# Kernel tuning notes

Hardware: AMD Instinct MI355X
Metric: run time of the kernel (lower is better)

## Reference

```python
import jax, jax.numpy as jnp
import numpy as np

NUM_BLOCKS = 8
WIDTH = 512
HIDDEN_SIZE_FACTOR = 1
HARD_THRESH_FRAC = 1.0
BLOCK_SIZE = WIDTH // NUM_BLOCKS


def setup_inputs() -> dict:
    key = jax.random.key(0)
    k_x, k1, k2, k3, k4 = jax.random.split(key, 5)
    B, L, P, C = 4, 2048, WIDTH, 8
    bs = BLOCK_SIZE
    hf = HIDDEN_SIZE_FACTOR
    scale = 1.0 / (bs * bs * hf)
    x = jax.random.normal(k_x, (B, L, P, C), dtype=jnp.float32)
    w1 = scale * jax.random.uniform(k1, (2, NUM_BLOCKS, bs, bs * hf), dtype=jnp.float32)
    b1 = scale * jax.random.uniform(k2, (2, NUM_BLOCKS, bs * hf), dtype=jnp.float32)
    w2 = scale * jax.random.uniform(k3, (2, NUM_BLOCKS, bs * hf, bs), dtype=jnp.float32)
    b2 = scale * jax.random.uniform(k4, (2, NUM_BLOCKS, bs), dtype=jnp.float32)
    return {"x": x, "w1": w1, "b1": b1, "w2": w2, "b2": b2}


def _gelu(v):
    # torch nn.GELU default is the exact (erf) variant
    return jax.nn.gelu(v, approximate=False)


def reference(x, w1, b1, w2, b2):
    B, L, P, C = x.shape
    nb, bs = NUM_BLOCKS, BLOCK_SIZE
    # rfft along L (norm='ortho'); complex64
    xf = jnp.fft.rfft(x, axis=1, norm="ortho")          # (B, Lf, P, C)
    Lf = xf.shape[1]
    xf = jnp.transpose(xf, (0, 1, 3, 2))                  # (B, Lf, C, P)
    xf = xf.reshape(B, Lf, C, nb, bs)                     # split P into blocks
    kept = int(Lf * HARD_THRESH_FRAC)
    xr, xi = jnp.real(xf[:, :kept]), jnp.imag(xf[:, :kept])
    # block-diagonal complex 2-layer MLP
    mm = lambda a, w: jnp.einsum("blcni,nio->blcno", a, w)
    o1r = _gelu(mm(xr, w1[0]) - mm(xi, w1[1]) + b1[0])
    o1i = _gelu(mm(xi, w1[0]) + mm(xr, w1[1]) + b1[1])
    o2r = mm(o1r, w2[0]) - mm(o1i, w2[1]) + b2[0]
    o2i = mm(o1i, w2[0]) + mm(o1r, w2[1]) + b2[1]
    # zero-pad the thresholded modes (no-op when kept == Lf)
    pad = Lf - kept
    if pad > 0:
        z = jnp.zeros((B, pad, C, nb, bs), dtype=o2r.dtype)
        o2r = jnp.concatenate([o2r, z], axis=1)
        o2i = jnp.concatenate([o2i, z], axis=1)
    xc = (o2r + 1j * o2i).reshape(B, Lf, C, P)
    out = jnp.fft.irfft(xc, n=L, axis=1, norm="ortho")  # (B, L, C, P)
    out = jnp.transpose(out, (0, 1, 3, 2))               # (B, L, P, C)
    return (out + x).astype(x.dtype)
```

## Files before the change

kernel.cpp:

```cpp
#include <hip/hip_runtime.h>
#include <hip/hip_bf16.h>

typedef unsigned short u16;
typedef unsigned int   u32;
typedef __bf16 bf16x8 __attribute__((ext_vector_type(8)));
typedef float  f32x4  __attribute__((ext_vector_type(4)));
typedef u32    u32x2  __attribute__((ext_vector_type(2)));

#define KPAD 1088
#define SEQ  1104
#define PI_F 3.14159265358979323846f
#define WAVE_FENCE() asm volatile("s_waitcnt lgkmcnt(0)" ::: "memory")

__device__ __forceinline__ u16 f2bf(float f){
    u32 u = __float_as_uint(f);
    return (u16)((u + 0x7FFFu + ((u >> 16) & 1u)) >> 16);
}
__device__ __forceinline__ float bf2f(u16 v){ return __uint_as_float(((u32)v) << 16); }
__device__ __forceinline__ int zmap2(int e){ return e + (e >> 4) + 4*(e >> 8); }

__device__ __forceinline__ int sig(int k){
    k &= 1023;
    int a = (k >> 6) + (((k >> 2) & 15) << 4) + ((k & 3) << 8);
    return zmap2(a);
}

__device__ __forceinline__ float2 cmul(float2 a, float2 b){
    return make_float2(a.x*b.x - a.y*b.y, a.x*b.y + a.y*b.x);
}
__device__ __forceinline__ void fft4v(float2& x0, float2& x1, float2& x2, float2& x3){
    float2 t0 = make_float2(x0.x+x2.x, x0.y+x2.y);
    float2 t1 = make_float2(x0.x-x2.x, x0.y-x2.y);
    float2 t2 = make_float2(x1.x+x3.x, x1.y+x3.y);
    float2 t3 = make_float2(x1.x-x3.x, x1.y-x3.y);
    x0 = make_float2(t0.x+t2.x, t0.y+t2.y);
    x2 = make_float2(t0.x-t2.x, t0.y-t2.y);
    x1 = make_float2(t1.x+t3.y, t1.y-t3.x);
    x3 = make_float2(t1.x-t3.y, t1.y+t3.x);
}
__device__ __forceinline__ void fft16(float2 a[16]){
    #pragma unroll
    for (int u1 = 0; u1 < 4; ++u1) fft4v(a[u1], a[u1+4], a[u1+8], a[u1+12]);
    const float Cq = 0.70710678118654752f;
    const float c1 = 0.92387953251128674f, s1 = 0.38268343236508977f;
    a[5]  = cmul(a[5],  make_float2(c1, -s1));
    a[6]  = cmul(a[6],  make_float2(Cq, -Cq));
    a[7]  = cmul(a[7],  make_float2(s1, -c1));
    a[9]  = cmul(a[9],  make_float2(Cq, -Cq));
    a[10] = cmul(a[10], make_float2(0.0f, -1.0f));
    a[11] = cmul(a[11], make_float2(-Cq, -Cq));
    a[13] = cmul(a[13], make_float2(s1, -c1));
    a[14] = cmul(a[14], make_float2(-Cq, -Cq));
    a[15] = cmul(a[15], make_float2(-c1, s1));
    #pragma unroll
    for (int ja = 0; ja < 4; ++ja) fft4v(a[4*ja], a[4*ja+1], a[4*ja+2], a[4*ja+3]);
}

__device__ __forceinline__ void fft_stepB_wave(float2* Z, int lane){
    int nA = lane & 15, jv = lane >> 4;
    float2 a[16];
    #pragma unroll
    for (int u = 0; u < 16; ++u) a[u] = Z[zmap2(nA + 16*u + 256*jv)];
    fft16(a);
    float s_, c_;
    __sincosf(-2.0f*PI_F*(float)(nA*jv)*(1.0f/1024.0f), &s_, &c_);
    float2 tw = make_float2(c_, s_);
    __sincosf(-2.0f*PI_F*(float)nA*(1.0f/256.0f), &s_, &c_);
    float2 st = make_float2(c_, s_);
    #pragma unroll
    for (int ju = 0; ju < 16; ++ju){
        Z[zmap2(nA + 16*ju + 256*jv)] = cmul(a[((ju&3)<<2)|(ju>>2)], tw);
        tw = cmul(tw, st);
    }
}
__device__ __forceinline__ void fft_stepC_wave(float2* Z, int lane){
    int ju = (lane & 63) >> 2, jv = lane & 3;
    float2 a[16];
    #pragma unroll
    for (int nA = 0; nA < 16; ++nA) a[nA] = Z[zmap2(nA + 16*ju + 256*jv)];
    fft16(a);
    #pragma unroll
    for (int kO = 0; kO < 16; ++kO)
        Z[zmap2(kO + 16*ju + 256*jv)] = a[((kO&3)<<2)|(kO>>2)];
}

__global__ __launch_bounds__(256) void prep_w(const float* __restrict__ w1,
                                              const float* __restrict__ w2,
                                              u16* __restrict__ WSW){
    int gid = blockIdx.x * 256 + threadIdx.x;
    int qd = gid >> 12;
    int t  = qd & 1;
    int n  = (qd >> 1) & 7;
    int l  = qd >> 4;
    int rr = gid & 4095;
    int o  = rr >> 6;
    int k  = rr & 63;
    const float* w = l ? w2 : w1;
    WSW[gid] = f2bf(w[((size_t)(t*8 + n)*64 + k)*64 + o]);
}


__device__ __forceinline__ u16 unpack_one(const float2* Zc, int k, int pl, float sf){
    float2 Zk = Zc[sig(k)], Zm = Zc[sig(1024 - k)];
    float sn_, cs_; __sincosf(PI_F*(float)k*(1.0f/1024.0f), &sn_, &cs_);
    float Er=0.5f*(Zk.x+Zm.x), Ei=0.5f*(Zk.y-Zm.y);
    float Dr=0.5f*(Zk.x-Zm.x), Di=0.5f*(Zk.y+Zm.y);
    float Xr = Er + cs_*Di - sn_*Dr;
    float Xi = Ei - sn_*Di - cs_*Dr;
    return f2bf((pl ? Xi : Xr) * sf);
}

__global__ __launch_bounds__(256) void fwd_fft(const float* __restrict__ X,
                                               u16* __restrict__ S){
    __shared__ float2 Zs[4*SEQ];
    int tid = threadIdx.x;
    int blk = blockIdx.x;
    int b = blk >> 10;
    int q = blk & 1023;
    int m8 = q & 7, tq = q >> 3;
    int Q = (tq >> 2)*8 + m8, s4 = tq & 3;
    int col0 = Q*16 + s4*4;
    int p  = col0 >> 3;
    int c0 = col0 & 7;
    int n  = p >> 6, pl_ = p & 63;
    int wave = tid >> 6, lane = tid & 63;

    float2 zz[4][4];
    #pragma unroll
    for (int v = 0; v < 4; ++v){
        int pi = tid + 256*v;
        size_t base = ((size_t)(b*2048 + 2*pi)*512 + p)*8 + c0;
        f32x4 ve = *(const f32x4*)(X + base);
        f32x4 vo = *(const f32x4*)(X + base + 4096);
        #pragma unroll
        for (int s = 0; s < 4; ++s) zz[v][s] = make_float2(ve[s], vo[s]);
    }
    {
        int u = (tid >> 4) & 15;
        float s_, c_;
        __sincosf(-2.0f*PI_F*(float)u*(1.0f/64.0f), &s_, &c_);
        float2 tw1 = make_float2(c_, s_);
        float2 tw2 = cmul(tw1, tw1);
        float2 tw3 = cmul(tw2, tw1);
        #pragma unroll
        for (int s = 0; s < 4; ++s){
            float2 x0 = zz[0][s], x1 = zz[1][s], x2 = zz[2][s], x3 = zz[3][s];
            fft4v(x0, x1, x2, x3);
            float2* Z = Zs + s*SEQ;
            Z[zmap2(tid)]     = x0;
            Z[zmap2(tid+256)] = cmul(x1, tw1);
            Z[zmap2(tid+512)] = cmul(x2, tw2);
            Z[zmap2(tid+768)] = cmul(x3, tw3);
        }
    }
    __syncthreads();
    float2* Z = Zs + wave*SEQ;
    fft_stepB_wave(Z, lane);
    WAVE_FENCE();
    fft_stepC_wave(Z, lane);
    WAVE_FENCE();
    const float sf = 0.02209708691207961f;
    int pl = lane >> 5, tr = lane & 31;
    u16* rp = S + (size_t)((((b*8 + (c0+wave))*8 + n)*2 + pl)*64 + pl_)*KPAD;
    for (int kk = tr*2; kk <= 1024; kk += 64){
        u16 w0 = unpack_one(Z, kk, pl, sf);
        if (kk < 1024){
            u16 w1 = unpack_one(Z, kk+1, pl, sf);
            *(u32*)(rp + kk) = (u32)w0 | ((u32)w1 << 16);
        } else {
            rp[kk] = w0;
        }
    }
}

__device__ __forceinline__ bf16x8 fetchB(const u16* mat, int o64, int k64, bool neg){
    const u32x2* pb = (const u32x2*)(mat + o64*68 + k64);
    u32x2 lo = pb[0], hi = pb[1];
    union { u32 u[4]; bf16x8 v; } bt;
    bt.u[0]=lo.x; bt.u[1]=lo.y; bt.u[2]=hi.x; bt.u[3]=hi.y;
    if (neg){ bt.u[0]^=0x80008000u; bt.u[1]^=0x80008000u; bt.u[2]^=0x80008000u; bt.u[3]^=0x80008000u; }
    return bt.v;
}
__device__ __forceinline__ bf16x8 loadU16x8(const u16* pp){
    union { u32 u[4]; bf16x8 v; } t;
    const u32* qq = (const u32*)pp;
    t.u[0]=qq[0]; t.u[1]=qq[1]; t.u[2]=qq[2]; t.u[3]=qq[3];
    return t.v;
}

__global__ __launch_bounds__(256) void mlp_kernel(const u16* __restrict__ WSW,
                                                  const float* __restrict__ b1,
                                                  const float* __restrict__ b2,
                                                  u16* __restrict__ S){
    __shared__ __align__(16) u16 AT[4][64*68];
    __shared__ __align__(16) u16 AS[8448];
    int tid = threadIdx.x;
    int blk = blockIdx.x;
    int n = blk & 7;
    int rest = blk >> 3;
    int t17 = rest % 17;
    int bc  = rest / 17;
    int b = bc >> 3, c = bc & 7;
    int k0 = t17 << 6;
    int lane = tid & 63, wv = tid >> 6;
    int lane15 = lane & 15, quad = lane >> 4;

    for (int mi = 0; mi < 4; ++mi){
        const u32* src = (const u32*)(WSW + (size_t)(((mi>>1)*8 + n)*2 + (mi&1))*4096);
        u32* dstm = (u32*)AT[mi];
        for (int d = tid; d < 2048; d += 256){
            int o = d >> 5, kk2 = d & 31;
            dstm[o*34 + kk2] = src[d];
        }
    }
    float bb1[8], bb2v[8];
    #pragma unroll
    for (int nb = 0; nb < 8; ++nb){
        int col = nb*16 + lane15;
        int tt = col >> 6, cc = col & 63;
        bb1[nb]  = b1[tt*512 + n*64 + cc];
        bb2v[nb] = b2[tt*512 + n*64 + cc];
    }
    size_t SB = (size_t)(((b*8 + c)*8 + n)*2)*64;
    {
        int rsub = tid & 31;
        for (int rr = tid >> 5; rr < 128; rr += 8){
            const u16* rp = S + (SB + rr)*KPAD + k0;
            u32 w = *(const u32*)(rp + 2*rsub);
            AS[(2*rsub)*132 + rr]   = (u16)(w & 0xFFFFu);
            AS[(2*rsub+1)*132 + rr] = (u16)(w >> 16);
        }
    }
    __syncthreads();
    const u16* arow = AS + (wv*16 + lane15)*132;
    bf16x8 afr[4];
    #pragma unroll
    for (int kb = 0; kb < 4; ++kb)
        afr[kb] = loadU16x8(arow + kb*32 + quad*8);
    f32x4 acc[8];
    #pragma unroll
    for (int nb = 0; nb < 8; ++nb){ acc[nb][0]=bb1[nb]; acc[nb][1]=bb1[nb]; acc[nb][2]=bb1[nb]; acc[nb][3]=bb1[nb]; }
    #pragma unroll
    for (int nb = 0; nb < 8; ++nb){
        int o64 = (nb&3)*16 + lane15;
        #pragma unroll
        for (int kb = 0; kb < 4; ++kb){
            int k64 = (kb&1)*32 + quad*8;
            const u16* mat; bool neg = false;
            if (kb < 2) mat = (nb<4) ? AT[0] : AT[1];
            else { if (nb<4){ mat = AT[1]; neg = true; } else mat = AT[0]; }
            acc[nb] = __builtin_amdgcn_mfma_f32_16x16x32_bf16(afr[kb], fetchB(mat,o64,k64,neg), acc[nb], 0,0,0);
        }
    }
    #pragma unroll
    for (int nb = 0; nb < 8; ++nb){
        #pragma unroll
        for (int r4 = 0; r4 < 4; ++r4){
            float xv = acc[nb][r4];
            float u_ = xv * 0.70710678118f;
            float u2 = u_*u_;
            float pg = 1.0f + u2*(-0.333333333f + u2*(0.1f + u2*(-0.0238095238f)));
            float h  = 0.5f * xv * (1.0f + 1.12837916709551f * u_ * pg);
            AS[(wv*16 + quad*4 + r4)*132 + nb*16 + lane15] = f2bf(h);
        }
    }
    bf16x8 a2[4];
    #pragma unroll
    for (int kb = 0; kb < 4; ++kb)
        a2[kb] = loadU16x8(arow + kb*32 + quad*8);
    f32x4 acc2[8];
    #pragma unroll
    for (int nb = 0; nb < 8; ++nb){ acc2[nb][0]=bb2v[nb]; acc2[nb][1]=bb2v[nb]; acc2[nb][2]=bb2v[nb]; acc2[nb][3]=bb2v[nb]; }
    #pragma unroll
    for (int nb = 0; nb < 8; ++nb){
        int o64 = (nb&3)*16 + lane15;
        #pragma unroll
        for (int kb = 0; kb < 4; ++kb){
            int k64 = (kb&1)*32 + quad*8;
            const u16* mat; bool neg = false;
            if (kb < 2) mat = (nb<4) ? AT[2] : AT[3];
            else { if (nb<4){ mat = AT[3]; neg = true; } else mat = AT[2]; }
            acc2[nb] = __builtin_amdgcn_mfma_f32_16x16x32_bf16(a2[kb], fetchB(mat,o64,k64,neg), acc2[nb], 0,0,0);
        }
    }
    __syncthreads();
    #pragma unroll
    for (int nb = 0; nb < 8; ++nb){
        #pragma unroll
        for (int r4 = 0; r4 < 4; ++r4)
            AS[(nb*16 + lane15)*66 + (wv*16 + quad*4 + r4)] = f2bf(acc2[nb][r4]);
    }
    __syncthreads();
    {
        int rsub = tid & 31;
        int k = k0 + 2*rsub;
        for (int rr = tid >> 5; rr < 128; rr += 8){
            u32 val = *(const u32*)(AS + rr*66 + 2*rsub);
            u16* rp = S + (SB + rr)*KPAD + k0;
            if (k + 1 <= 1024)  *(u32*)(rp + 2*rsub) = val;
            else if (k == 1024) rp[2*rsub] = (u16)(val & 0xFFFFu);
        }
    }
}

__global__ __launch_bounds__(256) void inv_fft(const u16* __restrict__ S,
                                               const float* __restrict__ X,
                                               float* __restrict__ OUT){
    __shared__ float2 Zs[4*SEQ];
    int tid = threadIdx.x;
    int blk = blockIdx.x;
    int b = blk >> 10;
    int q = blk & 1023;
    int m8 = q & 7, tq = q >> 3;
    int Q = (tq >> 2)*8 + m8, s4 = tq & 3;
    int col0 = Q*16 + s4*4;
    int p  = col0 >> 3;
    int c0 = col0 & 7;
    int n  = p >> 6, pl_ = p & 63;
    int wave = tid >> 6, lane = tid & 63;

    float2* Z = Zs + wave*SEQ;

    const u16* rpR = S + (size_t)((((b*8 + (c0+wave))*8 + n)*2 + 0)*64 + pl_)*KPAD;
    const u16* rpI = rpR + (size_t)64*KPAD;
    u32 wR[8], wI[8];
    #pragma unroll
    for (int i = 0; i < 8; ++i){
        wR[i] = *(const u32*)(rpR + 2*lane + 128*i);
        wI[i] = *(const u32*)(rpI + 2*lane + 128*i);
    }
    u16 nyq = rpR[1024];

    #pragma unroll
    for (int i = 0; i < 8; ++i){
        u32 od = (wR[i] >> 16) | (wI[i] & 0xFFFF0000u);
        Z[zmap2(2*lane + 1 + 128*(i&1) + 256*(i>>1))].x = __uint_as_float(od);
    }

    float er[8], ei[8];
    #pragma unroll
    for (int i = 0; i < 8; ++i){
        er[i] = bf2f((u16)(wR[i] & 0xFFFFu));
        ei[i] = bf2f((u16)(wI[i] & 0xFFFFu));
    }
    if (lane == 0) ei[0] = 0.0f;
    {
        float emr[8], emi[8];
        int srcE = (64 - lane) & 63;
        #pragma unroll
        for (int i = 0; i < 8; ++i){
            emr[i] = __shfl(er[7-i], srcE);
            emi[i] = __shfl(ei[7-i], srcE);
        }
        if (lane == 0){
            emr[0] = bf2f(nyq); emi[0] = 0.0f;
            #pragma unroll
            for (int i = 1; i < 8; ++i){ emr[i] = er[8-i]; emi[i] = ei[8-i]; }
        }
        #pragma unroll
        for (int i = 0; i < 8; ++i){
            float s2_, c2_;
            __sincosf(PI_F*(float)(2*lane + 128*i)*(1.0f/1024.0f), &s2_, &c2_);
            float Ex = 0.5f*(er[i] + emr[i]), Ey = 0.5f*(ei[i] - emi[i]);
            float Dx = 0.5f*(er[i] - emr[i]), Dy = 0.5f*(ei[i] + emi[i]);
            float Ox = c2_*Dx - s2_*Dy,      Oy = c2_*Dy + s2_*Dx;
            er[i] = Ex - Oy;  ei[i] = Ey + Ox;
        }
    }

    float2 twa1, twa2, twa3, twb1, twb2, twb3;
    {
        int u0 = lane >> 3;
        float su_, cu_;
        __sincosf(-2.0f*PI_F*(float)u0*(1.0f/64.0f), &su_, &cu_);
        twa1 = make_float2(cu_, su_);
        twa2 = cmul(twa1, twa1);
        twa3 = cmul(twa2, twa1);
        const float RH = 0.70710678118654752f;
        float2 rot = make_float2(RH, -RH);
        twb1 = cmul(twa1, rot);
        twb2 = cmul(twb1, twb1);
        twb3 = cmul(twb2, twb1);
    }
    #pragma unroll
    for (int j0 = 0; j0 < 2; ++j0){
        float2 t1 = j0 ? twb1 : twa1;
        float2 t2 = j0 ? twb2 : twa2;
        float2 t3 = j0 ? twb3 : twa3;
        int qb = 2*lane + 128*j0;
        float2 x0 = make_float2(er[j0],   ei[j0]);
        float2 x1 = make_float2(er[j0+2], ei[j0+2]);
        float2 x2 = make_float2(er[j0+4], ei[j0+4]);
        float2 x3 = make_float2(er[j0+6], ei[j0+6]);
        fft4v(x0, x1, x2, x3);
        Z[zmap2(qb)]     = x0;
        Z[zmap2(qb+256)] = cmul(x1, t1);
        Z[zmap2(qb+512)] = cmul(x2, t2);
        Z[zmap2(qb+768)] = cmul(x3, t3);
    }

    WAVE_FENCE();
    float odr[8], odi[8];
    #pragma unroll
    for (int i = 0; i < 8; ++i){
        u32 od = __float_as_uint(Z[zmap2(2*lane + 1 + 128*(i&1) + 256*(i>>1))].x);
        odr[i] = bf2f((u16)(od & 0xFFFFu));
        odi[i] = bf2f((u16)(od >> 16));
    }
    {
        float emr[8], emi[8];
        int srcO = 63 - lane;
        #pragma unroll
        for (int i = 0; i < 8; ++i){
            emr[i] = __shfl(odr[7-i], srcO);
            emi[i] = __shfl(odi[7-i], srcO);
        }
        #pragma unroll
        for (int i = 0; i < 8; ++i){
            float s2_, c2_;
            __sincosf(PI_F*(float)(2*lane + 1 + 128*i)*(1.0f/1024.0f), &s2_, &c2_);
            float Ex = 0.5f*(odr[i] + emr[i]), Ey = 0.5f*(odi[i] - emi[i]);
            float Dx = 0.5f*(odr[i] - emr[i]), Dy = 0.5f*(odi[i] + emi[i]);
            float Ox = c2_*Dx - s2_*Dy,        Oy = c2_*Dy + s2_*Dx;
            odr[i] = Ex - Oy;  odi[i] = Ey + Ox;
        }
    }

    #pragma unroll
    for (int j0 = 0; j0 < 2; ++j0){
        float2 t1 = j0 ? twb1 : twa1;
        float2 t2 = j0 ? twb2 : twa2;
        float2 t3 = j0 ? twb3 : twa3;
        int qb = 2*lane + 1 + 128*j0;
        float2 x0 = make_float2(odr[j0],   odi[j0]);
        float2 x1 = make_float2(odr[j0+2], odi[j0+2]);
        float2 x2 = make_float2(odr[j0+4], odi[j0+4]);
        float2 x3 = make_float2(odr[j0+6], odi[j0+6]);
        fft4v(x0, x1, x2, x3);
        Z[zmap2(qb)]     = x0;
        Z[zmap2(qb+256)] = cmul(x1, t1);
        Z[zmap2(qb+512)] = cmul(x2, t2);
        Z[zmap2(qb+768)] = cmul(x3, t3);
    }

    WAVE_FENCE();
    fft_stepB_wave(Z, lane);
    WAVE_FENCE();
    fft_stepC_wave(Z, lane);

    __builtin_amdgcn_sched_barrier(0);
    f32x4 xe[4], xo[4];
    #pragma unroll
    for (int i = 0; i < 4; ++i){
        int pi = tid + 256*i;
        size_t base = ((size_t)(b*2048 + 2*pi)*512 + p)*8 + c0;
        xe[i] = *(const f32x4*)(X + base);
        xo[i] = *(const f32x4*)(X + base + 4096);
    }

    __syncthreads();
    const float sc = 0.04419417382415922f;
    #pragma unroll
    for (int i = 0; i < 4; ++i){
        int pi = tid + 256*i;
        int zb = sig(1024 - pi);
        size_t base = ((size_t)(b*2048 + 2*pi)*512 + p)*8 + c0;
        f32x4 oe, oo;
        #pragma unroll
        for (int s = 0; s < 4; ++s){
            float2 r = Zs[s*SEQ + zb];
            oe[s] = r.x*sc + xe[i][s];
            oo[s] = r.y*sc + xo[i][s];
        }
        *(f32x4*)(OUT + base)        = oe;
        *(f32x4*)(OUT + base + 4096) = oo;
    }
}

extern "C" void kernel_launch(void* const* d_in, const int* in_sizes, int n_in,
                              void* d_out, int out_size, void* d_ws, size_t ws_size,
                              hipStream_t stream){
    (void)in_sizes; (void)n_in; (void)out_size; (void)ws_size;
    const float* x  = (const float*)d_in[0];
    const float* w1 = (const float*)d_in[1];
    const float* b1 = (const float*)d_in[2];
    const float* w2 = (const float*)d_in[3];
    const float* b2 = (const float*)d_in[4];
    float* out = (float*)d_out;
    u16* WSW = (u16*)d_ws;
    u16* S1  = (u16*)((char*)d_ws + (1 << 20));

    prep_w<<<dim3(512),  dim3(256), 0, stream>>>(w1, w2, WSW);
    fwd_fft<<<dim3(4096), dim3(256), 0, stream>>>(x, S1);
    mlp_kernel<<<dim3(4352), dim3(256), 0, stream>>>(WSW, b1, b2, S1);
    inv_fft<<<dim3(4096), dim3(256), 0, stream>>>(S1, x, out);
}
```

Baseline: 490.8 us.

## Process all 8 channels per FFT block with 512-thread blocks

The forward and inverse FFT kernels now handle all 8 channels of one (batch, P) column per block, using 512 threads and 8 waves instead of 256 threads covering 4 channels. Each row of 8 contiguous floats in X and OUT is therefore read or written in full by one block, giving 32-byte contiguous accesses instead of 16-byte half-rows split across blocks. The cost is twice the shared memory per block (8*SEQ float2) and larger blocks, which may lower occupancy or scheduling flexibility. The block index mapping changes to interleave P values.

```diff
diff --git a/kernel.cpp b/kernel.cpp
--- a/kernel.cpp
+++ b/kernel.cpp
@@ -110,33 +110,30 @@
     return f2bf((pl ? Xi : Xr) * sf);
 }
 
-__global__ __launch_bounds__(256) void fwd_fft(const float* __restrict__ X,
+
+__global__ __launch_bounds__(512) void fwd_fft(const float* __restrict__ X,
                                                u16* __restrict__ S){
-    __shared__ float2 Zs[4*SEQ];
+    __shared__ float2 Zs[8*SEQ];
     int tid = threadIdx.x;
     int blk = blockIdx.x;
-    int b = blk >> 10;
-    int q = blk & 1023;
-    int m8 = q & 7, tq = q >> 3;
-    int Q = (tq >> 2)*8 + m8, s4 = tq & 3;
-    int col0 = Q*16 + s4*4;
-    int p  = col0 >> 3;
-    int c0 = col0 & 7;
+    int b = blk >> 9;
+    int p = 2*(blk & 255) + ((blk >> 8) & 1);
     int n  = p >> 6, pl_ = p & 63;
     int wave = tid >> 6, lane = tid & 63;
+    int th = tid & 255, half = tid >> 8;
 
     float2 zz[4][4];
     #pragma unroll
     for (int v = 0; v < 4; ++v){
-        int pi = tid + 256*v;
-        size_t base = ((size_t)(b*2048 + 2*pi)*512 + p)*8 + c0;
+        int pi = th + 256*v;
+        size_t base = ((size_t)(b*2048 + 2*pi)*512 + p)*8 + half*4;
         f32x4 ve = *(const f32x4*)(X + base);
         f32x4 vo = *(const f32x4*)(X + base + 4096);
         #pragma unroll
         for (int s = 0; s < 4; ++s) zz[v][s] = make_float2(ve[s], vo[s]);
     }
     {
-        int u = (tid >> 4) & 15;
+        int u = (th >> 4) & 15;
         float s_, c_;
         __sincosf(-2.0f*PI_F*(float)u*(1.0f/64.0f), &s_, &c_);
         float2 tw1 = make_float2(c_, s_);
@@ -146,11 +143,11 @@
         for (int s = 0; s < 4; ++s){
             float2 x0 = zz[0][s], x1 = zz[1][s], x2 = zz[2][s], x3 = zz[3][s];
             fft4v(x0, x1, x2, x3);
-            float2* Z = Zs + s*SEQ;
-            Z[zmap2(tid)]     = x0;
-            Z[zmap2(tid+256)] = cmul(x1, tw1);
-            Z[zmap2(tid+512)] = cmul(x2, tw2);
-            Z[zmap2(tid+768)] = cmul(x3, tw3);
+            float2* Z = Zs + (half*4 + s)*SEQ;
+            Z[zmap2(th)]     = x0;
+            Z[zmap2(th+256)] = cmul(x1, tw1);
+            Z[zmap2(th+512)] = cmul(x2, tw2);
+            Z[zmap2(th+768)] = cmul(x3, tw3);
         }
     }
     __syncthreads();
@@ -161,7 +158,7 @@
     WAVE_FENCE();
     const float sf = 0.02209708691207961f;
     int pl = lane >> 5, tr = lane & 31;
-    u16* rp = S + (size_t)((((b*8 + (c0+wave))*8 + n)*2 + pl)*64 + pl_)*KPAD;
+    u16* rp = S + (size_t)((((b*8 + wave)*8 + n)*2 + pl)*64 + pl_)*KPAD;
     for (int kk = tr*2; kk <= 1024; kk += 64){
         u16 w0 = unpack_one(Z, kk, pl, sf);
         if (kk < 1024){
@@ -303,25 +300,20 @@
     }
 }
 
-__global__ __launch_bounds__(256) void inv_fft(const u16* __restrict__ S,
+__global__ __launch_bounds__(512) void inv_fft(const u16* __restrict__ S,
                                                const float* __restrict__ X,
                                                float* __restrict__ OUT){
-    __shared__ float2 Zs[4*SEQ];
+    __shared__ float2 Zs[8*SEQ];
     int tid = threadIdx.x;
     int blk = blockIdx.x;
-    int b = blk >> 10;
-    int q = blk & 1023;
-    int m8 = q & 7, tq = q >> 3;
-    int Q = (tq >> 2)*8 + m8, s4 = tq & 3;
-    int col0 = Q*16 + s4*4;
-    int p  = col0 >> 3;
-    int c0 = col0 & 7;
+    int b = blk >> 9;
+    int p = 2*(blk & 255) + ((blk >> 8) & 1);
     int n  = p >> 6, pl_ = p & 63;
     int wave = tid >> 6, lane = tid & 63;
 
     float2* Z = Zs + wave*SEQ;
 
-    const u16* rpR = S + (size_t)((((b*8 + (c0+wave))*8 + n)*2 + 0)*64 + pl_)*KPAD;
+    const u16* rpR = S + (size_t)((((b*8 + wave)*8 + n)*2 + 0)*64 + pl_)*KPAD;
     const u16* rpI = rpR + (size_t)64*KPAD;
     u32 wR[8], wI[8];
     #pragma unroll
@@ -449,31 +441,38 @@
     fft_stepC_wave(Z, lane);
 
     __builtin_amdgcn_sched_barrier(0);
-    f32x4 xe[4], xo[4];
-    #pragma unroll
-    for (int i = 0; i < 4; ++i){
-        int pi = tid + 256*i;
-        size_t base = ((size_t)(b*2048 + 2*pi)*512 + p)*8 + c0;
-        xe[i] = *(const f32x4*)(X + base);
-        xo[i] = *(const f32x4*)(X + base + 4096);
+    f32x4 xel[2], xeh[2], xol[2], xoh[2];
+    #pragma unroll
+    for (int i = 0; i < 2; ++i){
+        int pi = tid + 512*i;
+        size_t base = ((size_t)(b*2048 + 2*pi)*512 + p)*8;
+        xel[i] = *(const f32x4*)(X + base);
+        xeh[i] = *(const f32x4*)(X + base + 4);
+        xol[i] = *(const f32x4*)(X + base + 4096);
+        xoh[i] = *(const f32x4*)(X + base + 4100);
     }
 
     __syncthreads();
     const float sc = 0.04419417382415922f;
     #pragma unroll
-    for (int i = 0; i < 4; ++i){
-        int pi = tid + 256*i;
+    for (int i = 0; i < 2; ++i){
+        int pi = tid + 512*i;
         int zb = sig(1024 - pi);
-        size_t base = ((size_t)(b*2048 + 2*pi)*512 + p)*8 + c0;
-        f32x4 oe, oo;
+        size_t base = ((size_t)(b*2048 + 2*pi)*512 + p)*8;
+        f32x4 oel, oeh, ool, ooh;
         #pragma unroll
         for (int s = 0; s < 4; ++s){
-            float2 r = Zs[s*SEQ + zb];
-            oe[s] = r.x*sc + xe[i][s];
-            oo[s] = r.y*sc + xo[i][s];
-        }
-        *(f32x4*)(OUT + base)        = oe;
-        *(f32x4*)(OUT + base + 4096) = oo;
+            float2 r0 = Zs[s*SEQ + zb];
+            float2 r1 = Zs[(s+4)*SEQ + zb];
+            oel[s] = r0.x*sc + xel[i][s];
+            oeh[s] = r1.x*sc + xeh[i][s];
+            ool[s] = r0.y*sc + xol[i][s];
+            ooh[s] = r1.y*sc + xoh[i][s];
+        }
+        *(f32x4*)(OUT + base)        = oel;
+        *(f32x4*)(OUT + base + 4)    = oeh;
+        *(f32x4*)(OUT + base + 4096) = ool;
+        *(f32x4*)(OUT + base + 4100) = ooh;
     }
 }
 
@@ -491,7 +490,7 @@
     u16* S1  = (u16*)((char*)d_ws + (1 << 20));
 
     prep_w<<<dim3(512),  dim3(256), 0, stream>>>(w1, w2, WSW);
-    fwd_fft<<<dim3(4096), dim3(256), 0, stream>>>(x, S1);
+    fwd_fft<<<dim3(2048), dim3(512), 0, stream>>>(x, S1);
     mlp_kernel<<<dim3(4352), dim3(256), 0, stream>>>(WSW, b1, b2, S1);
-    inv_fft<<<dim3(4096), dim3(256), 0, stream>>>(S1, x, out);
-}
+    inv_fft<<<dim3(2048), dim3(512), 0, stream>>>(S1, x, out);
+}
```

Result: slower. 595.6 us (+21.3%).
